# Optimization experiments

Measured on AMD Instinct MI355X. Metric: run time of the kernel, lower is better.

The kernel has to match this reference:

```python
import jax, jax.numpy as jnp
import numpy as np

DIM = 192
NUM_HEADS = 6
WIN = (8, 8)
N = WIN[0] * WIN[1]  # 64 tokens per window


def _relative_position_index():
    ch = np.arange(WIN[0]); cw = np.arange(WIN[1])
    coords = np.stack(np.meshgrid(ch, cw, indexing='ij'))          # (2, Wh, Ww)
    flat = coords.reshape(2, -1)                                    # (2, N)
    rel = flat[:, :, None] - flat[:, None, :]                       # (2, N, N)
    rel = rel.transpose(1, 2, 0).copy()                             # (N, N, 2)
    rel[..., 0] += WIN[0] - 1
    rel[..., 1] += WIN[1] - 1
    rel[..., 0] *= 2 * WIN[1] - 1
    return jnp.asarray(rel.sum(-1), dtype=jnp.int32)                # (N, N)

RPI = _relative_position_index()


def setup_inputs() -> dict:
    key = jax.random.key(0)
    ks = jax.random.split(key, 20)
    B_, T, M, C = 128, 4, 4, DIM
    nW = 64
    x = jax.random.normal(ks[0], (B_, T, N, C), dtype=jnp.float32)
    x_kv = jax.random.normal(ks[1], (B_, M, N, C), dtype=jnp.float32)
    u = jax.random.uniform(ks[2], (nW, N, N))
    mask = jnp.where(u > 0.9, jnp.float32(-100.0), jnp.float32(0.0))
    s = 0.02
    p = lambda k, shape: jax.random.normal(k, shape, dtype=jnp.float32) * s
    return {
        'x': x, 'x_kv': x_kv, 'mask': mask,
        'rpb_table': p(ks[3], ((2 * WIN[0] - 1) * (2 * WIN[1] - 1), NUM_HEADS)),
        'q_w': p(ks[4], (C, C)), 'q_b': jnp.zeros((C,), jnp.float32),
        'kv_w': p(ks[5], (2 * C, C)), 'kv_b': jnp.zeros((2 * C,), jnp.float32),
        'pos_emb': jax.random.normal(ks[6], (N, C), dtype=jnp.float32) / C ** 0.5,
        'pq_w': p(ks[7], (C, C)), 'pq_b': jnp.zeros((C,), jnp.float32),
        'pk_w': p(ks[8], (C, C)), 'pk_b': jnp.zeros((C,), jnp.float32),
        'pv_w': p(ks[9], (C, C)), 'pv_b': jnp.zeros((C,), jnp.float32),
        'po_w': p(ks[10], (C, C)), 'po_b': jnp.zeros((C,), jnp.float32),
        'proj_w': p(ks[11], (C, C)), 'proj_b': jnp.zeros((C,), jnp.float32),
    }


def reference(x, x_kv, mask, rpb_table, q_w, q_b, kv_w, kv_b, pos_emb,
              pq_w, pq_b, pk_w, pk_b, pv_w, pv_b, po_w, po_b, proj_w, proj_b):
    B_, T, _, C = x.shape
    M = x_kv.shape[1]
    nH = NUM_HEADS
    hd = C // nH
    scale = hd ** -0.5

    # projections -> (B_, T, nH, N, hd) and (B_, M, nH, N, hd)
    q = (x @ q_w.T + q_b).reshape(B_, T, N, nH, hd).transpose(0, 1, 3, 2, 4)
    kv = (x_kv @ kv_w.T + kv_b).reshape(B_, M, N, 2, nH, hd)
    k = kv[:, :, :, 0].transpose(0, 1, 3, 2, 4)
    v = kv[:, :, :, 1].transpose(0, 1, 3, 2, 4)

    # scores: (B_, T, M, nH, N, N)
    attn = jnp.einsum('bthnd,bmhed->btmhne', q * scale, k)

    # relative position bias gather
    rpb = rpb_table[RPI.reshape(-1)].reshape(N, N, nH).transpose(2, 0, 1)
    attn = attn + rpb[None, None, None]

    # shifted-window mask (per window index within B_ = b * nW)
    nW = mask.shape[0]
    b = B_ // nW
    attn = attn.reshape(b, nW, T, M, nH, N, N) + mask[None, :, None, None, None]
    attn = attn.reshape(B_, T, M, nH, N, N)

    attn = jax.nn.softmax(attn, axis=-1)
    out = jnp.einsum('btmhne,bmhed->btmhnd', attn, v)
    # faithful to torch: transpose(1,2) then reshape (B_, T, M, N, C)
    out = jnp.swapaxes(out, 1, 2).reshape(B_, T, M, N, C)
    xp = out.reshape(B_ * T, M, N, C)

    # AttentionPooling1d over the M reference axis
    avg = xp.mean(axis=1, keepdims=True)
    xp = jnp.concatenate([avg, xp], axis=1) + pos_emb[None, None]   # (BT, M+1, N, C)
    BT = xp.shape[0]
    seq = xp.transpose(1, 2, 0, 3).reshape((M + 1) * N, BT, C)      # (m n) b c
    qq = (seq[:N] @ pq_w.T + pq_b).reshape(N, BT, nH, hd)
    kk = (seq @ pk_w.T + pk_b).reshape(-1, BT, nH, hd)
    vv = (seq @ pv_w.T + pv_b).reshape(-1, BT, nH, hd)
    a = jnp.einsum('qbhd,kbhd->bhqk', qq * scale, kk)
    a = jax.nn.softmax(a, axis=-1)
    o = jnp.einsum('bhqk,kbhd->qbhd', a, vv).reshape(N, BT, C)
    o = o @ po_w.T + po_b                                           # (N, BT, C)
    o = o.transpose(1, 0, 2).reshape(B_, T, N, C)

    o = jax.nn.gelu(o, approximate=False)
    return o @ proj_w.T + proj_b
```

## Files before the change

kernel.cpp:

```cpp
#include <hip/hip_runtime.h>
#include <math.h>


typedef float f32x4 __attribute__((ext_vector_type(4)));
typedef short s16x8 __attribute__((ext_vector_type(8)));
typedef unsigned short u16x4 __attribute__((ext_vector_type(4)));
typedef unsigned short u16x8 __attribute__((ext_vector_type(8)));

__device__ __forceinline__ unsigned short f2bf(float f) {
    union { float f; unsigned u; } c; c.f = f;
    return (unsigned short)((c.u + 0x7fffu + ((c.u >> 16) & 1u)) >> 16);
}
__device__ __forceinline__ float bf2f(unsigned short h) {
    union { unsigned u; float f; } c; c.u = ((unsigned)h) << 16;
    return c.f;
}

__global__ void wcvt_kernel(const float* __restrict__ q_w, const float* __restrict__ kv_w,
                            const float* __restrict__ pq_w, const float* __restrict__ pk_w,
                            const float* __restrict__ pv_w, const float* __restrict__ po_w,
                            const float* __restrict__ proj_w, unsigned short* __restrict__ wbf)
{
    int i = blockIdx.x * 256 + threadIdx.x;
    if (i >= 294912) return;
    const float* src; int off;
    if      (i < 36864)  { src = q_w;    off = 0; }
    else if (i < 110592) { src = kv_w;   off = 36864; }
    else if (i < 147456) { src = pq_w;   off = 110592; }
    else if (i < 184320) { src = pk_w;   off = 147456; }
    else if (i < 221184) { src = pv_w;   off = 184320; }
    else if (i < 258048) { src = po_w;   off = 221184; }
    else                 { src = proj_w; off = 258048; }
    wbf[i] = f2bf(src[i - off]);
}

__global__ void prep_kernel(const unsigned short* __restrict__ xp,
                            unsigned short* __restrict__ t0b)
{
    int i = blockIdx.x * 256 + threadIdx.x;
    int c8 = (i % 24) * 8;
    int n  = (i / 24) & 63;
    int bt = i / (24 * 64);
    float acc[8] = {0, 0, 0, 0, 0, 0, 0, 0};
    size_t base = (size_t)bt * 49152 + n * 192 + c8;
#pragma unroll
    for (int m = 0; m < 4; m++) {
        u16x8 v = *reinterpret_cast<const u16x8*>(&xp[base + m * 12288]);
#pragma unroll
        for (int e = 0; e < 8; e++) acc[e] += bf2f(v[e]);
    }
    u16x8 t;
#pragma unroll
    for (int e = 0; e < 8; e++) t[e] = f2bf(acc[e] * 0.25f);
    *reinterpret_cast<u16x8*>(&t0b[(size_t)(bt * 64 + n) * 192 + c8]) = t;
}

template <int SRC, int EPI, int OUTBF>
__global__ __launch_bounds__(256, 3)
void mgemm_kernel(const float* __restrict__ A, const unsigned short* __restrict__ Ab,
                  const unsigned short* __restrict__ Ab2,
                  const unsigned short* __restrict__ W0, const unsigned short* __restrict__ W1,
                  const float* __restrict__ b0, const float* __restrict__ b1,
                  void* __restrict__ C0v, void* __restrict__ C1v, int c0)
{
    __shared__ __align__(16) char As[128 * 192];
    __shared__ __align__(16) char Bs[96 * 192];
    const int tid = threadIdx.x;
    const int gm0 = blockIdx.x * 128;
    const int gn0 = blockIdx.y * 96;
    const int wid = tid >> 6;
    const int wm = wid >> 1, wn = wid & 1;
    const int lane = tid & 63;
    const int lr = lane & 15;
    const int lk = lane >> 4;

    const bool hiN = (gn0 >= 192);
    const unsigned short* Wsel = (EPI == 3 && hiN) ? W1 : W0;
    const int wrow0 = (EPI == 3 && hiN) ? (gn0 - 192) : gn0;

    f32x4 acc[4][3];
#pragma unroll
    for (int i = 0; i < 4; i++)
#pragma unroll
        for (int j = 0; j < 3; j++) acc[i][j] = (f32x4){0.f, 0.f, 0.f, 0.f};

    for (int kb = 0; kb < 192; kb += 96) {
        if (SRC == 0) {
#pragma unroll
            for (int it = 0; it < 12; it++) {
                int f4 = tid + it * 256;
                int row = f4 / 24;
                int kc4 = (f4 - row * 24) * 4;
                float4 v = *reinterpret_cast<const float4*>(
                    &A[(size_t)(gm0 + row) * 192 + kb + kc4]);
                u16x4 bvv;
                bvv[0] = f2bf(v.x); bvv[1] = f2bf(v.y);
                bvv[2] = f2bf(v.z); bvv[3] = f2bf(v.w);
                int boff = (kc4 * 2) ^ ((row & 3) << 4);
                *reinterpret_cast<u16x4*>(As + row * 192 + boff) = bvv;
            }
        } else {
#pragma unroll
            for (int it = 0; it < 6; it++) {
                int f8 = tid + it * 256;
                int row = f8 / 12;
                int c16 = f8 - row * 12;
                const unsigned short* src;
                if (SRC == 3) {
                    src = &Ab[(size_t)(gm0 + row) * 192 + kb + c16 * 8];
                } else {
                    int g = gm0 + row;
                    int bt = g / 320, tok = g - bt * 320; bt += c0;
                    src = (tok < 64)
                        ? &Ab2[(size_t)(bt * 64 + tok) * 192 + kb + c16 * 8]
                        : &Ab[(size_t)bt * 49152 + ((tok >> 6) - 1) * 12288
                              + (tok & 63) * 192 + kb + c16 * 8];
                }
                u16x8 v = *reinterpret_cast<const u16x8*>(src);
                int boff = (c16 * 16) ^ ((row & 3) << 4);
                *reinterpret_cast<u16x8*>(As + row * 192 + boff) = v;
            }
        }
        for (int f8 = tid; f8 < 1152; f8 += 256) {
            int row = f8 / 12;
            int c16 = f8 - row * 12;
            u16x8 v = *reinterpret_cast<const u16x8*>(
                &Wsel[(size_t)(wrow0 + row) * 192 + kb + c16 * 8]);
            int boff = (c16 * 16) ^ ((row & 3) << 4);
            *reinterpret_cast<u16x8*>(Bs + row * 192 + boff) = v;
        }
        __syncthreads();

#pragma unroll
        for (int ks = 0; ks < 3; ks++) {
            s16x8 af[4], bf[3];
#pragma unroll
            for (int i = 0; i < 4; i++) {
                int row = wm * 64 + i * 16 + lr;
                int off = (ks * 64 + lk * 16) ^ ((row & 3) << 4);
                af[i] = *reinterpret_cast<const s16x8*>(As + row * 192 + off);
            }
#pragma unroll
            for (int j = 0; j < 3; j++) {
                int row = wn * 48 + j * 16 + lr;
                int off = (ks * 64 + lk * 16) ^ ((row & 3) << 4);
                bf[j] = *reinterpret_cast<const s16x8*>(Bs + row * 192 + off);
            }
#pragma unroll
            for (int i = 0; i < 4; i++)
#pragma unroll
                for (int j = 0; j < 3; j++)
                    acc[i][j] = __builtin_amdgcn_mfma_f32_16x16x32_bf16(
                        af[i], bf[j], acc[i][j], 0, 0, 0);
        }
        __syncthreads();
    }

    if (OUTBF == 0) {
#pragma unroll
        for (int j = 0; j < 3; j++) {
            int bcol = gn0 + wn * 48 + j * 16 + lr;
            float bv = (EPI == 3 && bcol >= 192) ? b1[bcol - 192] : b0[bcol];
            float* dst = (float*)C0v;
            int oc = bcol;
            if ((EPI == 2 || EPI == 3) && bcol >= 192) { dst = (float*)C1v; oc = bcol - 192; }
#pragma unroll
            for (int i = 0; i < 4; i++) {
                int rbase = gm0 + wm * 64 + i * 16 + lk * 4;
#pragma unroll
                for (int r = 0; r < 4; r++) {
                    float v = acc[i][j][r] + bv;
                    if (EPI == 1) v = 0.5f * v * (1.f + erff(v * 0.70710678118654752440f));
                    dst[(size_t)(rbase + r) * 192 + oc] = v;
                }
            }
        }
    } else {
        unsigned short* As16 = (unsigned short*)As;
#pragma unroll
        for (int j = 0; j < 3; j++) {
            int bcol = gn0 + wn * 48 + j * 16 + lr;
            float bv = (EPI == 3 && bcol >= 192) ? b1[bcol - 192] : b0[bcol];
#pragma unroll
            for (int i = 0; i < 4; i++)
#pragma unroll
                for (int r = 0; r < 4; r++) {
                    float v = acc[i][j][r] + bv;
                    if (EPI == 1) v = 0.5f * v * (1.f + erff(v * 0.70710678118654752440f));
                    As16[(wm * 64 + i * 16 + lk * 4 + r) * 96 + wn * 48 + j * 16 + lr] = f2bf(v);
                }
        }
        __syncthreads();
        unsigned short* dst = (unsigned short*)((((EPI == 2) || (EPI == 3)) && hiN) ? C1v : C0v);
        const int oc0 = ((((EPI == 2) || (EPI == 3)) && hiN) ? gn0 - 192 : gn0);
#pragma unroll
        for (int it = 0; it < 6; it++) {
            int f8 = tid + it * 256;
            int row = f8 / 12, c16 = f8 - row * 12;
            u16x8 v = *reinterpret_cast<const u16x8*>(&As16[row * 96 + c16 * 8]);
            *reinterpret_cast<u16x8*>(&dst[(size_t)(gm0 + row) * 192 + oc0 + c16 * 8]) = v;
        }
    }
}

__global__ __launch_bounds__(768, 1)
void winattn_kernel(const float* __restrict__ qbuf,
                    const unsigned short* __restrict__ kbuf,
                    const unsigned short* __restrict__ vbuf,
                    const float* __restrict__ mask,
                    const float* __restrict__ rpbt, const float* __restrict__ pos,
                    unsigned short* __restrict__ xp)
{
    __shared__ float klds[64 * 192];
    __shared__ float vlds[64 * 192];
    __shared__ float mlds[64 * 65];
    __shared__ float rldsT[6 * 225];
    __shared__ float exm[768];
    __shared__ float exl[768];
    __shared__ unsigned obuf[6 * 64 * 17];
    const int tid = threadIdx.x;
    const int bid = blockIdx.x;
    const int bb = bid >> 2;
    const int m = bid & 3;
    const int w = tid >> 6;
    const int h = w >> 1;
    const int lane = tid & 63;

    const int kvbase = (bb * 4 + m) * 12288;
#pragma unroll
    for (int it = 0; it < 2; it++) {
        int i8 = tid + it * 768;
        u16x8 kq = *reinterpret_cast<const u16x8*>(&kbuf[kvbase + i8 * 8]);
        u16x8 vq = *reinterpret_cast<const u16x8*>(&vbuf[kvbase + i8 * 8]);
        f32x4 k0, k1, v0, v1;
#pragma unroll
        for (int e = 0; e < 4; e++) {
            k0[e] = bf2f(kq[e]); k1[e] = bf2f(kq[e + 4]);
            v0[e] = bf2f(vq[e]); v1[e] = bf2f(vq[e + 4]);
        }
        *reinterpret_cast<f32x4*>(&klds[i8 * 8]) = k0;
        *reinterpret_cast<f32x4*>(&klds[i8 * 8 + 4]) = k1;
        *reinterpret_cast<f32x4*>(&vlds[i8 * 8]) = v0;
        *reinterpret_cast<f32x4*>(&vlds[i8 * 8 + 4]) = v1;
    }
    const int widx = bb & 63;
    for (int f = tid; f < 4096; f += 768)
        mlds[(f >> 6) * 65 + (f & 63)] = mask[widx * 4096 + f];
    for (int f = tid; f < 1350; f += 768) {
        int hh = f / 225, rr = f - hh * 225;
        rldsT[f] = rpbt[rr * 6 + hh];
    }
    __syncthreads();

    const float scale = 0.17677669529663688110f;
    const int ni = lane >> 3, nj = lane & 7;
    const int e0 = (w & 1) << 5;

    for (int t = 0; t < 4; t++) {
        float qreg[32];
        const int qbase = ((bb * 4 + t) * 64 + lane) * 192 + h * 32;
#pragma unroll
        for (int j = 0; j < 8; j++) {
            float4 v = *reinterpret_cast<const float4*>(&qbuf[qbase + j * 4]);
            qreg[4 * j] = v.x; qreg[4 * j + 1] = v.y;
            qreg[4 * j + 2] = v.z; qreg[4 * j + 3] = v.w;
        }
        float s[32];
#pragma unroll
        for (int ee = 0; ee < 32; ee++) {
            int e = e0 + ee;
            const float4* kr = reinterpret_cast<const float4*>(&klds[e * 192 + h * 32]);
            float d0 = 0, d1 = 0, d2 = 0, d3 = 0;
#pragma unroll
            for (int q8 = 0; q8 < 8; q8++) {
                float4 k4 = kr[q8];
                d0 += qreg[q8 * 4] * k4.x;
                d1 += qreg[q8 * 4 + 1] * k4.y;
                d2 += qreg[q8 * 4 + 2] * k4.z;
                d3 += qreg[q8 * 4 + 3] * k4.w;
            }
            int ridx = (ni - (e >> 3) + 7) * 15 + (nj - (e & 7) + 7);
            s[ee] = (d0 + d1 + d2 + d3) * scale + rldsT[h * 225 + ridx] + mlds[lane * 65 + e];
        }
        float mrun = s[0];
#pragma unroll
        for (int ee = 1; ee < 32; ee++) mrun = fmaxf(mrun, s[ee]);
        float lrun = 0.f;
#pragma unroll
        for (int ee = 0; ee < 32; ee++) { s[ee] = __expf(s[ee] - mrun); lrun += s[ee]; }

        float o[32];
#pragma unroll
        for (int d = 0; d < 32; d++) o[d] = 0.f;
#pragma unroll
        for (int ee = 0; ee < 32; ee++) {
            float p = s[ee];
            const float4* vr = reinterpret_cast<const float4*>(&vlds[(e0 + ee) * 192 + h * 32]);
#pragma unroll
            for (int d8 = 0; d8 < 8; d8++) {
                float4 v4 = vr[d8];
                o[d8 * 4] += p * v4.x; o[d8 * 4 + 1] += p * v4.y;
                o[d8 * 4 + 2] += p * v4.z; o[d8 * 4 + 3] += p * v4.w;
            }
        }

        __syncthreads();
        exm[w * 64 + lane] = mrun;
        __syncthreads();
        float mo = exm[(w ^ 1) * 64 + lane];
        float mt = fmaxf(mrun, mo);
        float fs = __expf(mrun - mt);
        if (w & 1) {
            unsigned* ob = &obuf[h * 1088 + lane * 17];
#pragma unroll
            for (int j = 0; j < 16; j++) {
                unsigned lo = f2bf(fs * o[2 * j]);
                unsigned hi = f2bf(fs * o[2 * j + 1]);
                ob[j] = lo | (hi << 16);
            }
            exl[w * 64 + lane] = fs * lrun;
        }
        __syncthreads();
        if (!(w & 1)) {
            float lt = fs * lrun + exl[(w + 1) * 64 + lane];
            const float inv = 1.f / lt;
            const unsigned* ob = &obuf[h * 1088 + lane * 17];
            const int obase = bb * 196608 + m * 49152 + t * 12288 + h * 2048 + lane * 32;
#pragma unroll
            for (int j = 0; j < 8; j++) {
                unsigned p0 = ob[2 * j], p1 = ob[2 * j + 1];
                float4 pv = *reinterpret_cast<const float4*>(&pos[h * 2048 + lane * 32 + j * 4]);
                u16x4 v;
                v[0] = f2bf((fs * o[4 * j]     + bf2f((unsigned short)(p0 & 0xffff))) * inv + pv.x);
                v[1] = f2bf((fs * o[4 * j + 1] + bf2f((unsigned short)(p0 >> 16))) * inv + pv.y);
                v[2] = f2bf((fs * o[4 * j + 2] + bf2f((unsigned short)(p1 & 0xffff))) * inv + pv.z);
                v[3] = f2bf((fs * o[4 * j + 3] + bf2f((unsigned short)(p1 >> 16))) * inv + pv.w);
                *reinterpret_cast<u16x4*>(&xp[obase + j * 4]) = v;
            }
        }
    }
}

__global__ __launch_bounds__(320)
void poolattn3_kernel(const unsigned short* __restrict__ kk,
                      const unsigned short* __restrict__ vv,
                      const float* __restrict__ qq,
                      unsigned short* __restrict__ opool, int c0)
{
    __shared__ float ubuf[10560];
    __shared__ float scm[320], scl[320];
    const int tid = threadIdx.x;
    const int w = tid >> 6, lane = tid & 63;
    const int h = blockIdx.x, btl = blockIdx.y;
    const int bt = c0 + btl;
    float* Kf = ubuf + w * 2048;
    float* Vf = Kf + 1024;

    float qreg[32];
    const size_t qbase = (size_t)(bt * 64 + lane) * 192 + h * 32;
#pragma unroll
    for (int j = 0; j < 8; j++) {
        float4 v = *reinterpret_cast<const float4*>(&qq[qbase + j * 4]);
        qreg[4 * j] = v.x; qreg[4 * j + 1] = v.y;
        qreg[4 * j + 2] = v.z; qreg[4 * j + 3] = v.w;
    }
    const float scale = 0.17677669529663688110f;
    float mrun = -3.0e38f, lrun = 0.f;
    float o[32];
#pragma unroll
    for (int d = 0; d < 32; d++) o[d] = 0.f;

#pragma unroll
    for (int it = 0; it < 2; it++) {
        const int tt = w + it * 5;
        const unsigned short* ks = kk + (size_t)(btl * 320 + tt * 32) * 192 + h * 32;
        const unsigned short* vs = vv + (size_t)(btl * 320 + tt * 32) * 192 + h * 32;
#pragma unroll
        for (int ci = 0; ci < 2; ci++) {
            int idx = lane + ci * 64;
            int j = idx >> 2, q4 = (idx & 3) * 8;
            s16x8 kv8 = *reinterpret_cast<const s16x8*>(&ks[j * 192 + q4]);
            s16x8 vv8 = *reinterpret_cast<const s16x8*>(&vs[j * 192 + q4]);
            f32x4 lo, hi, vlo, vhi;
#pragma unroll
            for (int e = 0; e < 4; e++) {
                lo[e] = bf2f((unsigned short)kv8[e]);
                hi[e] = bf2f((unsigned short)kv8[e + 4]);
                vlo[e] = bf2f((unsigned short)vv8[e]);
                vhi[e] = bf2f((unsigned short)vv8[e + 4]);
            }
            *reinterpret_cast<f32x4*>(Kf + j * 32 + q4) = lo;
            *reinterpret_cast<f32x4*>(Kf + j * 32 + q4 + 4) = hi;
            *reinterpret_cast<f32x4*>(Vf + j * 32 + q4) = vlo;
            *reinterpret_cast<f32x4*>(Vf + j * 32 + q4 + 4) = vhi;
        }
        float s[32];
#pragma unroll
        for (int j = 0; j < 32; j++) {
            const float4* kr = reinterpret_cast<const float4*>(Kf + j * 32);
            float d0 = 0, d1 = 0, d2 = 0, d3 = 0;
#pragma unroll
            for (int q8 = 0; q8 < 8; q8++) {
                float4 k4 = kr[q8];
                d0 += qreg[q8 * 4] * k4.x;
                d1 += qreg[q8 * 4 + 1] * k4.y;
                d2 += qreg[q8 * 4 + 2] * k4.z;
                d3 += qreg[q8 * 4 + 3] * k4.w;
            }
            s[j] = (d0 + d1 + d2 + d3) * scale;
        }
        float mt = s[0];
#pragma unroll
        for (int j = 1; j < 32; j++) mt = fmaxf(mt, s[j]);
        float mnew = fmaxf(mrun, mt);
        float fct = __expf(mrun - mnew);
        lrun *= fct;
#pragma unroll
        for (int d = 0; d < 32; d++) o[d] *= fct;
#pragma unroll
        for (int j = 0; j < 32; j++) { float p = __expf(s[j] - mnew); lrun += p; s[j] = p; }
#pragma unroll
        for (int j = 0; j < 32; j++) {
            float p = s[j];
            const float4* vr = reinterpret_cast<const float4*>(Vf + j * 32);
#pragma unroll
            for (int d8 = 0; d8 < 8; d8++) {
                float4 v4 = vr[d8];
                o[d8 * 4] += p * v4.x; o[d8 * 4 + 1] += p * v4.y;
                o[d8 * 4 + 2] += p * v4.z; o[d8 * 4 + 3] += p * v4.w;
            }
        }
        mrun = mnew;
    }
    __syncthreads();
    scm[w * 64 + lane] = mrun;
    scl[w * 64 + lane] = lrun;
#pragma unroll
    for (int d = 0; d < 32; d++) ubuf[w * 2112 + lane * 33 + d] = o[d];
    __syncthreads();

    if (w == 0) {
        float m5 = scm[lane];
#pragma unroll
        for (int ww = 1; ww < 5; ww++) m5 = fmaxf(m5, scm[ww * 64 + lane]);
        float den = 0.f;
        float od[32];
#pragma unroll
        for (int d = 0; d < 32; d++) od[d] = 0.f;
#pragma unroll
        for (int ww = 0; ww < 5; ww++) {
            float f = __expf(scm[ww * 64 + lane] - m5);
            den += f * scl[ww * 64 + lane];
            const float* src = ubuf + ww * 2112 + lane * 33;
#pragma unroll
            for (int d = 0; d < 32; d++) od[d] += f * src[d];
        }
        const float inv = 1.f / den;
        const size_t ob = (size_t)(bt * 64 + lane) * 192 + h * 32;
#pragma unroll
        for (int j = 0; j < 8; j++) {
            u16x4 v;
            v[0] = f2bf(od[4 * j] * inv);     v[1] = f2bf(od[4 * j + 1] * inv);
            v[2] = f2bf(od[4 * j + 2] * inv); v[3] = f2bf(od[4 * j + 3] * inv);
            *reinterpret_cast<u16x4*>(&opool[ob + j * 4]) = v;
        }
    }
}

extern "C" void kernel_launch(void* const* d_in, const int* in_sizes, int n_in,
                              void* d_out, int out_size, void* d_ws, size_t ws_size,
                              hipStream_t stream) {
    (void)in_sizes; (void)n_in; (void)out_size; (void)ws_size;
    const float* x      = (const float*)d_in[0];
    const float* x_kv   = (const float*)d_in[1];
    const float* mask   = (const float*)d_in[2];
    const float* rpbt   = (const float*)d_in[3];
    const float* q_w    = (const float*)d_in[4];
    const float* q_b    = (const float*)d_in[5];
    const float* kv_w   = (const float*)d_in[6];
    const float* kv_b   = (const float*)d_in[7];
    const float* pos    = (const float*)d_in[8];
    const float* pq_w   = (const float*)d_in[9];
    const float* pq_b   = (const float*)d_in[10];
    const float* pk_w   = (const float*)d_in[11];
    const float* pk_b   = (const float*)d_in[12];
    const float* pv_w   = (const float*)d_in[13];
    const float* pv_b   = (const float*)d_in[14];
    const float* po_w   = (const float*)d_in[15];
    const float* po_b   = (const float*)d_in[16];
    const float* proj_w = (const float*)d_in[17];
    const float* proj_b = (const float*)d_in[18];
    float* out = (float*)d_out;
    char* ws = (char*)d_ws;

    float*          qbuf   = (float*)(ws);
    unsigned short* xp     = (unsigned short*)(ws + 25165824u);
    unsigned short* kbuf   = (unsigned short*)(ws + 75497472u);
    unsigned short* vbuf   = (unsigned short*)(ws + 88080384u);
    unsigned short* kkc    = (unsigned short*)(ws + 75497472u);
    unsigned short* vvc    = (unsigned short*)(ws + 106954752u);
    unsigned short* t0b    = (unsigned short*)(ws + 138412032u);
    unsigned short* opoolb = (unsigned short*)(ws + 150994944u);
    unsigned short* opob   = (unsigned short*)(ws + 163577856u);
    unsigned short* wbf    = (unsigned short*)(ws + 176160768u);
    float*          qq     = qbuf;

    dim3 blk(256);
    wcvt_kernel<<<1152, blk, 0, stream>>>(q_w, kv_w, pq_w, pk_w, pv_w, po_w, proj_w, wbf);
    mgemm_kernel<0, 0, 0><<<dim3(256, 2), blk, 0, stream>>>(
        x, nullptr, nullptr, wbf, nullptr, q_b, nullptr, qbuf, nullptr, 0);
    mgemm_kernel<0, 2, 1><<<dim3(256, 4), blk, 0, stream>>>(
        x_kv, nullptr, nullptr, wbf + 36864, nullptr, kv_b, nullptr, kbuf, vbuf, 0);
    winattn_kernel<<<512, 768, 0, stream>>>(qbuf, kbuf, vbuf, mask, rpbt, pos, xp);
    prep_kernel<<<3072, blk, 0, stream>>>(xp, t0b);
    mgemm_kernel<3, 0, 0><<<dim3(256, 2), blk, 0, stream>>>(
        nullptr, t0b, nullptr, wbf + 110592, nullptr, pq_b, nullptr, qq, nullptr, 0);
    for (int c0 = 0; c0 < 512; c0 += 256) {
        mgemm_kernel<4, 3, 1><<<dim3(640, 4), blk, 0, stream>>>(
            nullptr, xp, t0b, wbf + 147456, wbf + 184320, pk_b, pv_b, kkc, vvc, c0);
        poolattn3_kernel<<<dim3(6, 256), 320, 0, stream>>>(kkc, vvc, qq, opoolb, c0);
    }
    mgemm_kernel<3, 1, 1><<<dim3(256, 2), blk, 0, stream>>>(
        nullptr, opoolb, nullptr, wbf + 221184, nullptr, po_b, nullptr, opob, nullptr, 0);
    mgemm_kernel<3, 0, 0><<<dim3(256, 2), blk, 0, stream>>>(
        nullptr, opob, nullptr, wbf + 258048, nullptr, proj_b, nullptr, out, nullptr, 0);
}
```

Before: 626.3 us.

## Store pooling K/V head-major and parallelize pool-attention merge across four waves

The K/V projection GEMM now writes its output in a head-blocked layout (per head, rows of 32 contiguous elements), so each pool-attention block reads contiguous 32-row by 32-dim tiles instead of 64-byte strided slices of 384-byte rows. The pool-attention kernel moves the Q register load inside a non-unrolled loop to lower register pressure. Its final merge of the five partial softmax results is split across four waves, each producing 8 of the 32 output dims, instead of one wave doing all of it. The new layout adds index arithmetic to the GEMM store, and the merge step now reads strided LDS rows from more waves.

```diff
diff --git a/kernel.cpp b/kernel.cpp
--- a/kernel.cpp
+++ b/kernel.cpp
@@ -61,7 +61,7 @@
                   const unsigned short* __restrict__ Ab2,
                   const unsigned short* __restrict__ W0, const unsigned short* __restrict__ W1,
                   const float* __restrict__ b0, const float* __restrict__ b1,
-                  void* __restrict__ C0v, void* __restrict__ C1v, int c0)
+                  void* __restrict__ C0v, void* __restrict__ C1v, int c0, int hbs)
 {
     __shared__ __align__(16) char As[128 * 192];
     __shared__ __align__(16) char Bs[96 * 192];
@@ -198,7 +198,15 @@
             int f8 = tid + it * 256;
             int row = f8 / 12, c16 = f8 - row * 12;
             u16x8 v = *reinterpret_cast<const u16x8*>(&As16[row * 96 + c16 * 8]);
-            *reinterpret_cast<u16x8*>(&dst[(size_t)(gm0 + row) * 192 + oc0 + c16 * 8]) = v;
+            size_t idx;
+            if (hbs == 0) {
+                idx = (size_t)(gm0 + row) * 192 + oc0 + c16 * 8;
+            } else {
+                int col = oc0 + c16 * 8;
+                idx = (size_t)(col >> 5) * (size_t)hbs
+                    + (size_t)(gm0 + row) * 32 + (col & 31);
+            }
+            *reinterpret_cast<u16x8*>(&dst[idx]) = v;
         }
     }
 }
@@ -345,7 +353,7 @@
 void poolattn3_kernel(const unsigned short* __restrict__ kk,
                       const unsigned short* __restrict__ vv,
                       const float* __restrict__ qq,
-                      unsigned short* __restrict__ opool, int c0)
+                      unsigned short* __restrict__ opool, int c0, int hbs)
 {
     __shared__ float ubuf[10560];
     __shared__ float scm[320], scl[320];
@@ -356,43 +364,42 @@
     float* Kf = ubuf + w * 2048;
     float* Vf = Kf + 1024;
 
-    float qreg[32];
-    const size_t qbase = (size_t)(bt * 64 + lane) * 192 + h * 32;
-#pragma unroll
-    for (int j = 0; j < 8; j++) {
-        float4 v = *reinterpret_cast<const float4*>(&qq[qbase + j * 4]);
-        qreg[4 * j] = v.x; qreg[4 * j + 1] = v.y;
-        qreg[4 * j + 2] = v.z; qreg[4 * j + 3] = v.w;
-    }
     const float scale = 0.17677669529663688110f;
     float mrun = -3.0e38f, lrun = 0.f;
     float o[32];
 #pragma unroll
     for (int d = 0; d < 32; d++) o[d] = 0.f;
 
-#pragma unroll
+    const size_t qbase = (size_t)(bt * 64 + lane) * 192 + h * 32;
+    const size_t hb = (size_t)h * hbs;
+
+#pragma unroll 1
     for (int it = 0; it < 2; it++) {
         const int tt = w + it * 5;
-        const unsigned short* ks = kk + (size_t)(btl * 320 + tt * 32) * 192 + h * 32;
-        const unsigned short* vs = vv + (size_t)(btl * 320 + tt * 32) * 192 + h * 32;
+        const unsigned short* ks = kk + hb + ((size_t)btl * 320 + tt * 32) * 32;
+        const unsigned short* vs = vv + hb + ((size_t)btl * 320 + tt * 32) * 32;
 #pragma unroll
         for (int ci = 0; ci < 2; ci++) {
-            int idx = lane + ci * 64;
-            int j = idx >> 2, q4 = (idx & 3) * 8;
-            s16x8 kv8 = *reinterpret_cast<const s16x8*>(&ks[j * 192 + q4]);
-            s16x8 vv8 = *reinterpret_cast<const s16x8*>(&vs[j * 192 + q4]);
+            int i8 = lane + ci * 64;
+            u16x8 kv8 = *reinterpret_cast<const u16x8*>(&ks[i8 * 8]);
+            u16x8 vv8 = *reinterpret_cast<const u16x8*>(&vs[i8 * 8]);
             f32x4 lo, hi, vlo, vhi;
 #pragma unroll
             for (int e = 0; e < 4; e++) {
-                lo[e] = bf2f((unsigned short)kv8[e]);
-                hi[e] = bf2f((unsigned short)kv8[e + 4]);
-                vlo[e] = bf2f((unsigned short)vv8[e]);
-                vhi[e] = bf2f((unsigned short)vv8[e + 4]);
-            }
-            *reinterpret_cast<f32x4*>(Kf + j * 32 + q4) = lo;
-            *reinterpret_cast<f32x4*>(Kf + j * 32 + q4 + 4) = hi;
-            *reinterpret_cast<f32x4*>(Vf + j * 32 + q4) = vlo;
-            *reinterpret_cast<f32x4*>(Vf + j * 32 + q4 + 4) = vhi;
+                lo[e] = bf2f(kv8[e]);  hi[e] = bf2f(kv8[e + 4]);
+                vlo[e] = bf2f(vv8[e]); vhi[e] = bf2f(vv8[e + 4]);
+            }
+            *reinterpret_cast<f32x4*>(Kf + i8 * 8) = lo;
+            *reinterpret_cast<f32x4*>(Kf + i8 * 8 + 4) = hi;
+            *reinterpret_cast<f32x4*>(Vf + i8 * 8) = vlo;
+            *reinterpret_cast<f32x4*>(Vf + i8 * 8 + 4) = vhi;
+        }
+        float qreg[32];
+#pragma unroll
+        for (int j = 0; j < 8; j++) {
+            float4 v = *reinterpret_cast<const float4*>(&qq[qbase + j * 4]);
+            qreg[4 * j] = v.x; qreg[4 * j + 1] = v.y;
+            qreg[4 * j + 2] = v.z; qreg[4 * j + 3] = v.w;
         }
         float s[32];
 #pragma unroll
@@ -439,31 +446,30 @@
     for (int d = 0; d < 32; d++) ubuf[w * 2112 + lane * 33 + d] = o[d];
     __syncthreads();
 
-    if (w == 0) {
-        float m5 = scm[lane];
-#pragma unroll
-        for (int ww = 1; ww < 5; ww++) m5 = fmaxf(m5, scm[ww * 64 + lane]);
+    if (tid < 256) {
+        const int q = tid & 63, grp = tid >> 6;
+        float m5 = scm[q];
+#pragma unroll
+        for (int ww = 1; ww < 5; ww++) m5 = fmaxf(m5, scm[ww * 64 + q]);
         float den = 0.f;
-        float od[32];
-#pragma unroll
-        for (int d = 0; d < 32; d++) od[d] = 0.f;
+        float od[8];
+#pragma unroll
+        for (int e = 0; e < 8; e++) od[e] = 0.f;
 #pragma unroll
         for (int ww = 0; ww < 5; ww++) {
-            float f = __expf(scm[ww * 64 + lane] - m5);
-            den += f * scl[ww * 64 + lane];
-            const float* src = ubuf + ww * 2112 + lane * 33;
-#pragma unroll
-            for (int d = 0; d < 32; d++) od[d] += f * src[d];
+            float f = __expf(scm[ww * 64 + q] - m5);
+            den += f * scl[ww * 64 + q];
+            const float* src = ubuf + ww * 2112 + q * 33 + grp * 8;
+#pragma unroll
+            for (int e = 0; e < 8; e++) od[e] += f * src[e];
         }
         const float inv = 1.f / den;
-        const size_t ob = (size_t)(bt * 64 + lane) * 192 + h * 32;
-#pragma unroll
-        for (int j = 0; j < 8; j++) {
-            u16x4 v;
-            v[0] = f2bf(od[4 * j] * inv);     v[1] = f2bf(od[4 * j + 1] * inv);
-            v[2] = f2bf(od[4 * j + 2] * inv); v[3] = f2bf(od[4 * j + 3] * inv);
-            *reinterpret_cast<u16x4*>(&opool[ob + j * 4]) = v;
-        }
+        const size_t ob = (size_t)(bt * 64 + q) * 192 + h * 32 + grp * 8;
+        u16x4 v0, v1;
+#pragma unroll
+        for (int e = 0; e < 4; e++) { v0[e] = f2bf(od[e] * inv); v1[e] = f2bf(od[e + 4] * inv); }
+        *reinterpret_cast<u16x4*>(&opool[ob]) = v0;
+        *reinterpret_cast<u16x4*>(&opool[ob + 4]) = v1;
     }
 }
 
@@ -504,24 +510,25 @@
     unsigned short* opob   = (unsigned short*)(ws + 163577856u);
     unsigned short* wbf    = (unsigned short*)(ws + 176160768u);
     float*          qq     = qbuf;
+    const int HBS = 256 * 320 * 32;
 
     dim3 blk(256);
     wcvt_kernel<<<1152, blk, 0, stream>>>(q_w, kv_w, pq_w, pk_w, pv_w, po_w, proj_w, wbf);
     mgemm_kernel<0, 0, 0><<<dim3(256, 2), blk, 0, stream>>>(
-        x, nullptr, nullptr, wbf, nullptr, q_b, nullptr, qbuf, nullptr, 0);
+        x, nullptr, nullptr, wbf, nullptr, q_b, nullptr, qbuf, nullptr, 0, 0);
     mgemm_kernel<0, 2, 1><<<dim3(256, 4), blk, 0, stream>>>(
-        x_kv, nullptr, nullptr, wbf + 36864, nullptr, kv_b, nullptr, kbuf, vbuf, 0);
+        x_kv, nullptr, nullptr, wbf + 36864, nullptr, kv_b, nullptr, kbuf, vbuf, 0, 0);
     winattn_kernel<<<512, 768, 0, stream>>>(qbuf, kbuf, vbuf, mask, rpbt, pos, xp);
     prep_kernel<<<3072, blk, 0, stream>>>(xp, t0b);
     mgemm_kernel<3, 0, 0><<<dim3(256, 2), blk, 0, stream>>>(
-        nullptr, t0b, nullptr, wbf + 110592, nullptr, pq_b, nullptr, qq, nullptr, 0);
+        nullptr, t0b, nullptr, wbf + 110592, nullptr, pq_b, nullptr, qq, nullptr, 0, 0);
     for (int c0 = 0; c0 < 512; c0 += 256) {
         mgemm_kernel<4, 3, 1><<<dim3(640, 4), blk, 0, stream>>>(
-            nullptr, xp, t0b, wbf + 147456, wbf + 184320, pk_b, pv_b, kkc, vvc, c0);
-        poolattn3_kernel<<<dim3(6, 256), 320, 0, stream>>>(kkc, vvc, qq, opoolb, c0);
+            nullptr, xp, t0b, wbf + 147456, wbf + 184320, pk_b, pv_b, kkc, vvc, c0, HBS);
+        poolattn3_kernel<<<dim3(6, 256), 320, 0, stream>>>(kkc, vvc, qq, opoolb, c0, HBS);
     }
     mgemm_kernel<3, 1, 1><<<dim3(256, 2), blk, 0, stream>>>(
-        nullptr, opoolb, nullptr, wbf + 221184, nullptr, po_b, nullptr, opob, nullptr, 0);
+        nullptr, opoolb, nullptr, wbf + 221184, nullptr, po_b, nullptr, opob, nullptr, 0, 0);
     mgemm_kernel<3, 0, 0><<<dim3(256, 2), blk, 0, stream>>>(
-        nullptr, opob, nullptr, wbf + 258048, nullptr, proj_b, nullptr, out, nullptr, 0);
-}
+        nullptr, opob, nullptr, wbf + 258048, nullptr, proj_b, nullptr, out, nullptr, 0, 0);
+}
```

Measured after the change: 600.9 us, median of 2. 1.04x faster.
